# Kernel optimization log

Hardware: AMD Instinct MI355X
Metric: run time of the kernel (lower is better)

## Reference

```python
import jax, jax.numpy as jnp
import numpy as np

N, E, IN, ED, HID, B, K = 50000, 800000, 128, 64, 256, 128, 1000


def setup_inputs() -> dict:
    key = jax.random.key(0)
    ks = jax.random.split(key, 16)

    def lin(k, fi, fo):
        k1, k2 = jax.random.split(k)
        s = 1.0 / np.sqrt(fi)
        return (jax.random.uniform(k1, (fi, fo), jnp.float32, -s, s),
                jax.random.uniform(k2, (fo,), jnp.float32, -s, s))

    We, be = lin(ks[0], ED, IN)        # GINEConv edge projection edge_dim -> in_channels
    W1, b1 = lin(ks[1], IN, HID)       # GINE nn layer 1
    W2, b2 = lin(ks[2], HID, HID)      # GINE nn layer 2
    Wg1, bg1 = lin(ks[3], HID, 128)    # gate_nn layer 1
    Wg2, bg2 = lin(ks[4], 128, 1)      # gate_nn layer 2
    Wh, bh = lin(ks[5], HID, K)        # head

    x = jax.random.normal(ks[6], (N, IN), jnp.float32)
    edge_index = jax.random.randint(ks[7], (2, E), 0, N, jnp.int64)
    edge_attr = jax.random.normal(ks[8], (E, ED), jnp.float32)
    batch = jnp.sort(jax.random.randint(ks[9], (N,), 0, B, jnp.int64))

    return {"x": x, "edge_index": edge_index, "edge_attr": edge_attr, "batch": batch,
            "We": We, "be": be, "W1": W1, "b1": b1, "W2": W2, "b2": b2,
            "Wg1": Wg1, "bg1": bg1, "Wg2": Wg2, "bg2": bg2, "Wh": Wh, "bh": bh}


def reference(x, edge_index, edge_attr, batch, We, be, W1, b1, W2, b2,
              Wg1, bg1, Wg2, bg2, Wh, bh):
    src, dst = edge_index[0], edge_index[1]
    # GINEConv message: ReLU(x_j + Lin(edge_attr)), scatter-add to dst (eps=0)
    e = edge_attr @ We + be                      # [E, IN]
    m = jax.nn.relu(x[src] + e)                  # [E, IN]
    agg = jax.ops.segment_sum(m, dst, num_segments=N)  # [N, IN]
    h = x + agg                                  # (1+eps)*x + agg, eps=0
    h = jax.nn.relu(h @ W1 + b1) @ W2 + b2       # [N, HID]
    # GlobalAttention: segment softmax of gate over graphs, weighted sum
    gate = jax.nn.relu(h @ Wg1 + bg1) @ Wg2 + bg2            # [N, 1]
    gmax = jax.ops.segment_max(gate, batch, num_segments=B)  # [B, 1]
    a = jnp.exp(gate - gmax[batch])
    denom = jax.ops.segment_sum(a, batch, num_segments=B)    # [B, 1]
    attn = a / denom[batch]
    pooled = jax.ops.segment_sum(attn * h, batch, num_segments=B)  # [B, HID]
    logits = pooled @ Wh + bh                    # [B, K]
    return (logits, pooled)
```

## Files before the change

### kernel.cpp

```cpp
#include <hip/hip_runtime.h>
#include <stdint.h>

#define NN    50000
#define EE    800000
#define IN_C  128
#define ED_C  64
#define HID_C 256
#define BB    128
#define KK    1000
#define G1_C  128
#define NV    50176


typedef __attribute__((ext_vector_type(8))) short bfrag;
typedef __attribute__((ext_vector_type(4))) float f4acc;

__device__ __forceinline__ unsigned short f2bs(float f){
  unsigned u = __float_as_uint(f);
  return (unsigned short)((u + 0x7fffu + ((u >> 16) & 1u)) >> 16);
}
__device__ __forceinline__ float bs2f(unsigned short s){
  return __uint_as_float(((unsigned)s) << 16);
}

__device__ __forceinline__ void atomicMaxFloat(float* addr, float val){
  int old = __float_as_int(*addr);
  while (__int_as_float(old) < val){
    int assumed = old;
    old = atomicCAS((int*)addr, assumed, __float_as_int(val));
    if (old == assumed) break;
  }
}

__global__ __launch_bounds__(256) void k_prep(
    const float* __restrict__ We, const float* __restrict__ W1,
    const float* __restrict__ W2, const float* __restrict__ Wg1,
    unsigned short* __restrict__ Wet, unsigned short* __restrict__ W1t,
    unsigned short* __restrict__ W2t, unsigned short* __restrict__ Wg1t)
{
  int i = blockIdx.x * 256 + threadIdx.x;
  if (i < 128 * 64){ int c = i >> 6, k = i & 63;  Wet[i]  = f2bs(We[k * 128 + c]); }
  if (i < 256 * 128){ int n = i >> 7, k = i & 127; W1t[i]  = f2bs(W1[k * 256 + n]); }
  if (i < 256 * 256){ int n = i >> 8, k = i & 255; W2t[i]  = f2bs(W2[k * 256 + n]); }
  if (i < 128 * 256){ int n = i >> 8, k = i & 255; Wg1t[i] = f2bs(Wg1[k * 128 + n]); }
}

__global__ __launch_bounds__(256) void k_init(float* __restrict__ agg,
                                              int* __restrict__ cnt,
                                              int* __restrict__ fill,
                                              int* __restrict__ aux,
                                              float* __restrict__ gmax,
                                              float* __restrict__ denom,
                                              float* __restrict__ pooled){
  size_t i = (size_t)blockIdx.x * 256 + threadIdx.x;
  if (i < (size_t)NN * IN_C) agg[i] = 0.f;
  if (i < NV){ cnt[i] = 0; fill[i] = 0; }
  if (i < 256) aux[i] = 0;
  if (i < BB){ gmax[i] = -1e30f; denom[i] = 0.f; }
  if (i < BB * HID_C) pooled[i] = 0.f;
}

__global__ __launch_bounds__(256) void k_hist(const int* __restrict__ ei,
                                              int* __restrict__ cnt){
  int e = blockIdx.x * 256 + threadIdx.x;
  if (e < EE) atomicAdd(&cnt[ei[EE + e]], 1);
}

__global__ __launch_bounds__(256) void k_scan1(const int* __restrict__ cnt,
                                               int* __restrict__ off,
                                               int* __restrict__ aux){
  __shared__ int s[256];
  int t = threadIdx.x, i = blockIdx.x * 256 + t;
  int val = cnt[i];
  s[t] = val; __syncthreads();
#pragma unroll
  for (int o = 1; o < 256; o <<= 1){
    int v = (t >= o) ? s[t - o] : 0;
    __syncthreads();
    s[t] += v;
    __syncthreads();
  }
  off[i] = s[t] - val;
  if (t == 255) aux[blockIdx.x] = s[255];
}

__global__ __launch_bounds__(256) void k_scan2(int* __restrict__ aux){
  __shared__ int s[256];
  int t = threadIdx.x;
  int val = aux[t];
  s[t] = val; __syncthreads();
#pragma unroll
  for (int o = 1; o < 256; o <<= 1){
    int v = (t >= o) ? s[t - o] : 0;
    __syncthreads();
    s[t] += v;
    __syncthreads();
  }
  aux[t] = s[t] - val;
}

__global__ __launch_bounds__(256) void k_scan3(int* __restrict__ off,
                                               const int* __restrict__ aux){
  int i = blockIdx.x * 256 + threadIdx.x;
  off[i] += aux[blockIdx.x];
}

__global__ __launch_bounds__(256) void k_scatter(const int* __restrict__ ei,
                                                 const int* __restrict__ off,
                                                 int* __restrict__ fill,
                                                 uint4* __restrict__ sorted){
  int e = blockIdx.x * 256 + threadIdx.x;
  if (e < EE){
    int s = ei[e], d = ei[EE + e];
    int pos = off[d] + atomicAdd(&fill[d], 1);
    sorted[pos] = make_uint4((unsigned)e, (unsigned)s, (unsigned)d, 0u);
  }
}

__global__ __launch_bounds__(256, 4) void k_edge2(
    const float* __restrict__ x, const uint4* __restrict__ sorted,
    const float* __restrict__ edge_attr,
    const unsigned short* __restrict__ Wet, const float* __restrict__ be,
    float* __restrict__ agg)
{
  __shared__ float msgS[64 * 132];
  __shared__ uint4 sE[64];
  __shared__ int runStart[66];
  __shared__ int nRunsS;
  unsigned short* eaS = (unsigned short*)msgS;

  const int tid = threadIdx.x;
  const int e0 = blockIdx.x * 64;
  if (tid < 64) sE[tid] = sorted[e0 + tid];
  __syncthreads();

  const int lane = tid & 63, wv = tid >> 6;
  const int q = lane >> 4, l15 = lane & 15;
  const int g0 = wv * 16;

  const int xrow = g0 + (lane >> 2);
  const int xc0 = (lane & 3) * 32;
  const float* xptr = x + (size_t)((int)sE[xrow].y) * IN_C + xc0;
  float4 xr[8];
#pragma unroll
  for (int j = 0; j < 8; ++j) xr[j] = *(const float4*)(xptr + j * 4);

#pragma unroll
  for (int t = 0; t < 4; ++t){
    int f4 = t * 256 + tid;
    int er = f4 >> 4;
    int kk = (f4 & 15) * 4;
    int eid = (int)sE[er].x;
    const float4 v = *(const float4*)(edge_attr + (size_t)eid * ED_C + kk);
    unsigned p0 = (unsigned)f2bs(v.x) | ((unsigned)f2bs(v.y) << 16);
    unsigned p1 = (unsigned)f2bs(v.z) | ((unsigned)f2bs(v.w) << 16);
    *(uint2*)&eaS[er * 72 + kk] = make_uint2(p0, p1);
  }

  if (tid < 64){
    bool flag = (tid == 0) || ((int)sE[tid].z != (int)sE[tid - 1].z);
    unsigned long long m = __ballot(flag);
    int pre = __popcll(m & ((1ull << tid) - 1ull));
    if ((m >> tid) & 1ull) runStart[pre] = tid;
    if (tid == 0){
      int nr = __popcll(m);
      nRunsS = nr;
      runStart[nr] = 64;
    }
  }
  __syncthreads();

  f4acc acc[8];
  const f4acc zz = {0.f, 0.f, 0.f, 0.f};
#pragma unroll
  for (int nt = 0; nt < 8; ++nt) acc[nt] = zz;

#pragma unroll
  for (int ks = 0; ks < 2; ++ks){
    bfrag a = *(const bfrag*)&eaS[(g0 + l15) * 72 + ks * 32 + q * 8];
#pragma unroll
    for (int nt = 0; nt < 8; ++nt){
      int c = nt * 16 + l15;
      bfrag b = *(const bfrag*)(Wet + c * ED_C + ks * 32 + q * 8);
      acc[nt] = __builtin_amdgcn_mfma_f32_16x16x32_bf16(a, b, acc[nt], 0, 0, 0);
    }
  }

  float bev[8];
#pragma unroll
  for (int nt = 0; nt < 8; ++nt) bev[nt] = be[nt * 16 + l15];

  __syncthreads();

#pragma unroll
  for (int nt = 0; nt < 8; ++nt){
    int c = nt * 16 + l15;
#pragma unroll
    for (int r = 0; r < 4; ++r)
      msgS[(g0 + q * 4 + r) * 132 + c] = acc[nt][r] + bev[nt];
  }

  {
    float* mr = &msgS[xrow * 132 + xc0];
#pragma unroll
    for (int j = 0; j < 8; ++j){
      float4 w = *(float4*)(mr + j * 4);
      const float4 v = xr[j];
      w.x = fmaxf(w.x + v.x, 0.f);
      w.y = fmaxf(w.y + v.y, 0.f);
      w.z = fmaxf(w.z + v.z, 0.f);
      w.w = fmaxf(w.w + v.w, 0.f);
      *(float4*)(mr + j * 4) = w;
    }
  }
  __syncthreads();

  {
    const int col = tid & 127;
    const int h = tid >> 7;
    const int nR = nRunsS;
    for (int i = h; i < nR; i += 2){
      int s = runStart[i], e = runStart[i + 1];
      int dst = (int)sE[s].z;
      float run = 0.f;
      for (int r = s; r < e; ++r) run += msgS[r * 132 + col];
      size_t a = (size_t)dst * IN_C + col;
      if (s == 0 || e == 64) atomicAdd(&agg[a], run);
      else                   agg[a] = run;
    }
  }
}

__global__ __launch_bounds__(256) void k_h0(const float* __restrict__ agg,
                                            const float* __restrict__ x,
                                            unsigned short* __restrict__ h0b){
  int i = blockIdx.x * 256 + threadIdx.x;
  if (i < NN * IN_C) h0b[i] = f2bs(agg[i] + x[i]);
}

template<int K, bool RELU, bool OF32, bool OB16>
__global__ __launch_bounds__(256) void k_gemm(
    const unsigned short* __restrict__ A, const unsigned short* __restrict__ Wt,
    const float* __restrict__ bias, float* __restrict__ outf,
    unsigned short* __restrict__ outb, int M, int Ntot)
{
  __shared__ unsigned short aS[64 * 40];
  __shared__ unsigned short bS[128 * 40];
  const int tid = threadIdx.x;
  const int lane = tid & 63, wv = tid >> 6;
  const int wi = wv >> 1, wj = wv & 1;
  const int q = lane >> 4, l15 = lane & 15;
  const int mb0 = blockIdx.x * 64;
  const int nb0 = blockIdx.y * 128;
  const int arow = tid >> 2, achk = tid & 3;

  f4acc acc[2][4];
  const f4acc zz = {0.f, 0.f, 0.f, 0.f};
#pragma unroll
  for (int mt = 0; mt < 2; ++mt)
#pragma unroll
    for (int nt = 0; nt < 4; ++nt) acc[mt][nt] = zz;

  for (int ks = 0; ks < K / 32; ++ks){
    {
      int m = mb0 + arow; if (m >= M) m = M - 1;
      const uint4 v = *(const uint4*)(A + (size_t)m * K + ks * 32 + achk * 8);
      *(uint4*)&aS[arow * 40 + achk * 8] = v;
    }
#pragma unroll
    for (int i = 0; i < 2; ++i){
      int idx = i * 256 + tid;
      int row = idx >> 2, chk = idx & 3;
      const uint4 v = *(const uint4*)(Wt + (size_t)(nb0 + row) * K + ks * 32 + chk * 8);
      *(uint4*)&bS[row * 40 + chk * 8] = v;
    }
    __syncthreads();
    bfrag a[2], b[4];
#pragma unroll
    for (int mt = 0; mt < 2; ++mt)
      a[mt] = *(const bfrag*)&aS[(wi * 32 + mt * 16 + l15) * 40 + q * 8];
#pragma unroll
    for (int nt = 0; nt < 4; ++nt)
      b[nt] = *(const bfrag*)&bS[(wj * 64 + nt * 16 + l15) * 40 + q * 8];
#pragma unroll
    for (int mt = 0; mt < 2; ++mt)
#pragma unroll
      for (int nt = 0; nt < 4; ++nt)
        acc[mt][nt] = __builtin_amdgcn_mfma_f32_16x16x32_bf16(a[mt], b[nt], acc[mt][nt], 0, 0, 0);
    __syncthreads();
  }

  const int mb = mb0 + wi * 32;
  const int nb = nb0 + wj * 64;
#pragma unroll
  for (int nt = 0; nt < 4; ++nt){
    int c = nb + nt * 16 + l15;
    float bv = bias[c];
#pragma unroll
    for (int mt = 0; mt < 2; ++mt){
#pragma unroll
      for (int r = 0; r < 4; ++r){
        int m = mb + mt * 16 + q * 4 + r;
        if (m < M){
          float v = acc[mt][nt][r] + bv;
          if (RELU) v = v > 0.f ? v : 0.f;
          if (OF32) outf[(size_t)m * Ntot + c] = v;
          if (OB16) outb[(size_t)m * Ntot + c] = f2bs(v);
        }
      }
    }
  }
}

__global__ __launch_bounds__(256) void k_gate2(const float* __restrict__ g1,
                                               const float* __restrict__ Wg2,
                                               const float* __restrict__ bg2,
                                               float* __restrict__ gate, int nrows){
  const int lane = threadIdx.x & 63, wv = threadIdx.x >> 6;
  const float2 w2 = *(const float2*)(Wg2 + lane * 2);
  const float bg = bg2[0];
  for (int r = blockIdx.x * 4 + wv; r < nrows; r += gridDim.x * 4){
    const float2 a2 = *(const float2*)(g1 + (size_t)r * G1_C + lane * 2);
    float p = a2.x * w2.x + a2.y * w2.y;
#pragma unroll
    for (int off = 32; off > 0; off >>= 1) p += __shfl_down(p, off);
    if (lane == 0) gate[r] = p + bg;
  }
}

__global__ __launch_bounds__(256) void k_gmax(const float* __restrict__ gate,
                                              const int* __restrict__ batch,
                                              float* __restrict__ gmax, int nrows){
  __shared__ float red[256];
  const int tid = threadIdx.x;
  const int n0 = blockIdx.x * 256;
  const int n = n0 + tid;
  const int nlast = (n0 + 255 < nrows) ? n0 + 255 : nrows - 1;
  const int bmin = batch[n0], bmax = batch[nlast];
  float val = -3e38f; int b = bmax;
  if (n < nrows){ b = batch[n]; val = gate[n]; }
  for (int bb = bmin; bb <= bmax; ++bb){
    red[tid] = (b == bb) ? val : -3e38f;
    __syncthreads();
    for (int s = 128; s > 0; s >>= 1){
      if (tid < s) red[tid] = fmaxf(red[tid], red[tid + s]);
      __syncthreads();
    }
    if (tid == 0 && red[0] > -1e37f) atomicMaxFloat(&gmax[bb], red[0]);
    __syncthreads();
  }
}

__global__ __launch_bounds__(256) void k_expsum(const float* __restrict__ gate,
                                                const int* __restrict__ batch,
                                                const float* __restrict__ gmax,
                                                float* __restrict__ aexp,
                                                float* __restrict__ denom, int nrows){
  __shared__ float red[256];
  const int tid = threadIdx.x;
  const int n0 = blockIdx.x * 256;
  const int n = n0 + tid;
  const int nlast = (n0 + 255 < nrows) ? n0 + 255 : nrows - 1;
  const int bmin = batch[n0], bmax = batch[nlast];
  float val = 0.f; int b = bmax;
  if (n < nrows){
    b = batch[n];
    val = expf(gate[n] - gmax[b]);
    aexp[n] = val;
  }
  for (int bb = bmin; bb <= bmax; ++bb){
    red[tid] = (b == bb) ? val : 0.f;
    __syncthreads();
    for (int s = 128; s > 0; s >>= 1){
      if (tid < s) red[tid] += red[tid + s];
      __syncthreads();
    }
    if (tid == 0 && red[0] != 0.f) atomicAdd(&denom[bb], red[0]);
    __syncthreads();
  }
}

__global__ __launch_bounds__(256) void k_pool(const unsigned short* __restrict__ h2b,
                                              const float* __restrict__ aexp,
                                              const float* __restrict__ denom,
                                              const int* __restrict__ batch,
                                              float* __restrict__ pooled, int nrows){
  const int c = threadIdx.x;
  const int n0 = blockIdx.x * 256;
  int n1 = n0 + 256; if (n1 > nrows) n1 = nrows;
  float acc = 0.f;
  int curb = batch[n0];
  for (int n = n0; n < n1; ++n){
    int b = batch[n];
    if (b != curb){
      atomicAdd(&pooled[(size_t)curb * HID_C + c], acc);
      acc = 0.f; curb = b;
    }
    float wgt = aexp[n] / denom[b];
    acc = fmaf(wgt, bs2f(h2b[(size_t)n * HID_C + c]), acc);
  }
  atomicAdd(&pooled[(size_t)curb * HID_C + c], acc);
}

__global__ __launch_bounds__(256) void k_head(const float* __restrict__ pooled,
                                              const float* __restrict__ Wh,
                                              const float* __restrict__ bh,
                                              float* __restrict__ out_logits,
                                              float* __restrict__ out_pooled){
  __shared__ float p[HID_C];
  const int b = blockIdx.x, t = threadIdx.x;
  float pv = pooled[(size_t)b * HID_C + t];
  p[t] = pv;
  out_pooled[(size_t)b * HID_C + t] = pv;
  __syncthreads();
  for (int c = t; c < KK; c += 256){
    float acc = bh[c];
#pragma unroll 8
    for (int k = 0; k < HID_C; ++k)
      acc = fmaf(p[k], Wh[k * KK + c], acc);
    out_logits[(size_t)b * KK + c] = acc;
  }
}

extern "C" void kernel_launch(void* const* d_in, const int* in_sizes, int n_in,
                              void* d_out, int out_size, void* d_ws, size_t ws_size,
                              hipStream_t stream) {
  const float* x   = (const float*)d_in[0];
  const int*   ei  = (const int*)d_in[1];
  const float* ea  = (const float*)d_in[2];
  const int*   batch = (const int*)d_in[3];
  const float* We  = (const float*)d_in[4];
  const float* be  = (const float*)d_in[5];
  const float* W1  = (const float*)d_in[6];
  const float* b1  = (const float*)d_in[7];
  const float* W2  = (const float*)d_in[8];
  const float* b2  = (const float*)d_in[9];
  const float* Wg1 = (const float*)d_in[10];
  const float* bg1 = (const float*)d_in[11];
  const float* Wg2 = (const float*)d_in[12];
  const float* bg2 = (const float*)d_in[13];
  const float* Wh  = (const float*)d_in[14];
  const float* bh  = (const float*)d_in[15];

  float* out_logits = (float*)d_out;
  float* out_pooled = out_logits + (size_t)BB * KK;

  float* agg    = (float*)d_ws;
  float* gate   = agg   + (size_t)NN * IN_C;
  float* aexp   = gate  + NN;
  float* gmax   = aexp  + NN;
  float* denom  = gmax  + BB;
  float* pooled = denom + BB;
  float* fend   = pooled + (size_t)BB * HID_C;
  unsigned short* h0b  = (unsigned short*)fend;
  unsigned short* h1b  = h0b + (size_t)NN * IN_C;
  unsigned short* h2b  = h1b + (size_t)NN * HID_C;
  unsigned short* Wet  = h2b + (size_t)NN * HID_C;
  unsigned short* W1t  = Wet + 128 * 64;
  unsigned short* W2t  = W1t + 256 * 128;
  unsigned short* Wg1t = W2t + 256 * 256;
  float* g1f = agg;
  uint4* sorted = (uint4*)h1b;
  int* cnt  = (int*)(sorted + EE);
  int* off  = cnt + NV;
  int* fill = off + NV;
  int* aux  = fill + NV;

  k_prep<<<256, 256, 0, stream>>>(We, W1, W2, Wg1, Wet, W1t, W2t, Wg1t);
  k_init<<<(NN * IN_C + 255) / 256, 256, 0, stream>>>(agg, cnt, fill, aux, gmax, denom, pooled);
  k_hist   <<<(EE + 255) / 256, 256, 0, stream>>>(ei, cnt);
  k_scan1  <<<NV / 256, 256, 0, stream>>>(cnt, off, aux);
  k_scan2  <<<1, 256, 0, stream>>>(aux);
  k_scan3  <<<NV / 256, 256, 0, stream>>>(off, aux);
  k_scatter<<<(EE + 255) / 256, 256, 0, stream>>>(ei, off, fill, sorted);
  k_edge2<<<EE / 64, 256, 0, stream>>>(x, sorted, ea, Wet, be, agg);
  k_h0<<<(NN * IN_C + 255) / 256, 256, 0, stream>>>(agg, x, h0b);
  k_gemm<128, true,  false, true ><<<dim3(782, 2), 256, 0, stream>>>(h0b, W1t, b1, (float*)0, h1b, NN, HID_C);
  k_gemm<256, false, false, true ><<<dim3(782, 2), 256, 0, stream>>>(h1b, W2t, b2, (float*)0, h2b, NN, HID_C);
  k_gemm<256, true,  true,  false><<<dim3(782, 1), 256, 0, stream>>>(h2b, Wg1t, bg1, g1f, (unsigned short*)0, NN, G1_C);
  k_gate2<<<3125, 256, 0, stream>>>(g1f, Wg2, bg2, gate, NN);
  k_gmax  <<<(NN + 255) / 256, 256, 0, stream>>>(gate, batch, gmax, NN);
  k_expsum<<<(NN + 255) / 256, 256, 0, stream>>>(gate, batch, gmax, aexp, denom, NN);
  k_pool  <<<(NN + 255) / 256, 256, 0, stream>>>(h2b, aexp, denom, batch, pooled, NN);
  k_head<<<BB, 256, 0, stream>>>(pooled, Wh, bh, out_logits, out_pooled);
}
```

Baseline: 751.0 us.

## Pre-permute edge attributes to bf16 in destination-sorted order during scatter

The scatter pass now writes each edge's attributes, converted to bf16, into a destination-sorted buffer alongside a compact (src,dst) pair. The edge-message kernel then reads the attribute tile contiguously, with no per-edge fp32 gather or conversion inside the MFMA projection. This removes the indirect fp32 edge_attr reads from the edge kernel, but adds an extra full-size bf16 write and read of the edge attributes. The new path runs only when the workspace is large enough; otherwise the old path is kept.

```diff
diff --git a/kernel.cpp b/kernel.cpp
--- a/kernel.cpp
+++ b/kernel.cpp
@@ -117,6 +117,26 @@
   }
 }
 
+__global__ __launch_bounds__(256) void k_scatter2(
+    const int* __restrict__ ei, const float* __restrict__ ea,
+    const int* __restrict__ off, int* __restrict__ fill,
+    uint2* __restrict__ sd, unsigned short* __restrict__ EA)
+{
+  int e = blockIdx.x * 256 + threadIdx.x;
+  if (e >= EE) return;
+  int s = ei[e], d = ei[EE + e];
+  int pos = off[d] + atomicAdd(&fill[d], 1);
+  sd[pos] = make_uint2((unsigned)s, (unsigned)d);
+  const float4* s4 = (const float4*)(ea + (size_t)e * ED_C);
+  uint2* d2 = (uint2*)(EA + (size_t)pos * ED_C);
+#pragma unroll
+  for (int j = 0; j < 16; ++j){
+    float4 v = s4[j];
+    d2[j] = make_uint2((unsigned)f2bs(v.x) | ((unsigned)f2bs(v.y) << 16),
+                       (unsigned)f2bs(v.z) | ((unsigned)f2bs(v.w) << 16));
+  }
+}
+
 __global__ __launch_bounds__(256, 4) void k_edge2(
     const float* __restrict__ x, const uint4* __restrict__ sorted,
     const float* __restrict__ edge_attr,
@@ -222,6 +242,104 @@
     for (int i = h; i < nR; i += 2){
       int s = runStart[i], e = runStart[i + 1];
       int dst = (int)sE[s].z;
+      float run = 0.f;
+      for (int r = s; r < e; ++r) run += msgS[r * 132 + col];
+      size_t a = (size_t)dst * IN_C + col;
+      if (s == 0 || e == 64) atomicAdd(&agg[a], run);
+      else                   agg[a] = run;
+    }
+  }
+}
+
+__global__ __launch_bounds__(256, 4) void k_edge3(
+    const float* __restrict__ x, const uint2* __restrict__ sd,
+    const unsigned short* __restrict__ EA,
+    const unsigned short* __restrict__ Wet, const float* __restrict__ be,
+    float* __restrict__ agg)
+{
+  __shared__ float msgS[64 * 132];
+  __shared__ uint2 sE[64];
+  __shared__ int runStart[66];
+  __shared__ int nRunsS;
+
+  const int tid = threadIdx.x;
+  if (tid < 64) sE[tid] = sd[(size_t)blockIdx.x * 64 + tid];
+  __syncthreads();
+
+  const int lane = tid & 63, wv = tid >> 6;
+  const int q = lane >> 4, l15 = lane & 15;
+  const int g0 = wv * 16;
+
+  const int xrow = g0 + (lane >> 2);
+  const int xc0 = (lane & 3) * 32;
+  const float* xptr = x + (size_t)((int)sE[xrow].x) * IN_C + xc0;
+  float4 xr[8];
+#pragma unroll
+  for (int j = 0; j < 8; ++j) xr[j] = *(const float4*)(xptr + j * 4);
+
+  if (tid < 64){
+    bool flag = (tid == 0) || (sE[tid].y != sE[tid - 1].y);
+    unsigned long long m = __ballot(flag);
+    int pre = __popcll(m & ((1ull << tid) - 1ull));
+    if ((m >> tid) & 1ull) runStart[pre] = tid;
+    if (tid == 0){
+      int nr = __popcll(m);
+      nRunsS = nr;
+      runStart[nr] = 64;
+    }
+  }
+
+  const unsigned short* EAb = EA + (size_t)blockIdx.x * 64 * ED_C;
+  f4acc acc[8];
+  const f4acc zz = {0.f, 0.f, 0.f, 0.f};
+#pragma unroll
+  for (int nt = 0; nt < 8; ++nt) acc[nt] = zz;
+
+#pragma unroll
+  for (int ks = 0; ks < 2; ++ks){
+    bfrag a = *(const bfrag*)(EAb + (size_t)(g0 + l15) * ED_C + ks * 32 + q * 8);
+#pragma unroll
+    for (int nt = 0; nt < 8; ++nt){
+      int c = nt * 16 + l15;
+      bfrag b = *(const bfrag*)(Wet + c * ED_C + ks * 32 + q * 8);
+      acc[nt] = __builtin_amdgcn_mfma_f32_16x16x32_bf16(a, b, acc[nt], 0, 0, 0);
+    }
+  }
+
+  float bev[8];
+#pragma unroll
+  for (int nt = 0; nt < 8; ++nt) bev[nt] = be[nt * 16 + l15];
+
+#pragma unroll
+  for (int nt = 0; nt < 8; ++nt){
+    int c = nt * 16 + l15;
+#pragma unroll
+    for (int r = 0; r < 4; ++r)
+      msgS[(g0 + q * 4 + r) * 132 + c] = acc[nt][r] + bev[nt];
+  }
+
+  {
+    float* mr = &msgS[xrow * 132 + xc0];
+#pragma unroll
+    for (int j = 0; j < 8; ++j){
+      float4 w = *(float4*)(mr + j * 4);
+      const float4 v = xr[j];
+      w.x = fmaxf(w.x + v.x, 0.f);
+      w.y = fmaxf(w.y + v.y, 0.f);
+      w.z = fmaxf(w.z + v.z, 0.f);
+      w.w = fmaxf(w.w + v.w, 0.f);
+      *(float4*)(mr + j * 4) = w;
+    }
+  }
+  __syncthreads();
+
+  {
+    const int col = tid & 127;
+    const int h = tid >> 7;
+    const int nR = nRunsS;
+    for (int i = h; i < nR; i += 2){
+      int s = runStart[i], e = runStart[i + 1];
+      int dst = (int)sE[s].y;
       float run = 0.f;
       for (int r = s; r < e; ++r) run += msgS[r * 132 + col];
       size_t a = (size_t)dst * IN_C + col;
@@ -452,35 +570,75 @@
   float* denom  = gmax  + BB;
   float* pooled = denom + BB;
   float* fend   = pooled + (size_t)BB * HID_C;
-  unsigned short* h0b  = (unsigned short*)fend;
-  unsigned short* h1b  = h0b + (size_t)NN * IN_C;
-  unsigned short* h2b  = h1b + (size_t)NN * HID_C;
-  unsigned short* Wet  = h2b + (size_t)NN * HID_C;
-  unsigned short* W1t  = Wet + 128 * 64;
-  unsigned short* W2t  = W1t + 256 * 128;
-  unsigned short* Wg1t = W2t + 256 * 256;
   float* g1f = agg;
-  uint4* sorted = (uint4*)h1b;
-  int* cnt  = (int*)(sorted + EE);
-  int* off  = cnt + NV;
-  int* fill = off + NV;
-  int* aux  = fill + NV;
-
-  k_prep<<<256, 256, 0, stream>>>(We, W1, W2, Wg1, Wet, W1t, W2t, Wg1t);
-  k_init<<<(NN * IN_C + 255) / 256, 256, 0, stream>>>(agg, cnt, fill, aux, gmax, denom, pooled);
-  k_hist   <<<(EE + 255) / 256, 256, 0, stream>>>(ei, cnt);
-  k_scan1  <<<NV / 256, 256, 0, stream>>>(cnt, off, aux);
-  k_scan2  <<<1, 256, 0, stream>>>(aux);
-  k_scan3  <<<NV / 256, 256, 0, stream>>>(off, aux);
-  k_scatter<<<(EE + 255) / 256, 256, 0, stream>>>(ei, off, fill, sorted);
-  k_edge2<<<EE / 64, 256, 0, stream>>>(x, sorted, ea, Wet, be, agg);
-  k_h0<<<(NN * IN_C + 255) / 256, 256, 0, stream>>>(agg, x, h0b);
-  k_gemm<128, true,  false, true ><<<dim3(782, 2), 256, 0, stream>>>(h0b, W1t, b1, (float*)0, h1b, NN, HID_C);
-  k_gemm<256, false, false, true ><<<dim3(782, 2), 256, 0, stream>>>(h1b, W2t, b2, (float*)0, h2b, NN, HID_C);
-  k_gemm<256, true,  true,  false><<<dim3(782, 1), 256, 0, stream>>>(h2b, Wg1t, bg1, g1f, (unsigned short*)0, NN, G1_C);
-  k_gate2<<<3125, 256, 0, stream>>>(g1f, Wg2, bg2, gate, NN);
-  k_gmax  <<<(NN + 255) / 256, 256, 0, stream>>>(gate, batch, gmax, NN);
-  k_expsum<<<(NN + 255) / 256, 256, 0, stream>>>(gate, batch, gmax, aexp, denom, NN);
-  k_pool  <<<(NN + 255) / 256, 256, 0, stream>>>(h2b, aexp, denom, batch, pooled, NN);
-  k_head<<<BB, 256, 0, stream>>>(pooled, Wh, bh, out_logits, out_pooled);
-}
+
+  const size_t NEED_BIG = 136000000ULL;
+
+  if (ws_size >= NEED_BIG){
+    unsigned short* Wet  = (unsigned short*)fend;
+    unsigned short* W1t  = Wet + 128 * 64;
+    unsigned short* W2t  = W1t + 256 * 128;
+    unsigned short* Wg1t = W2t + 256 * 256;
+    unsigned short* wend = Wg1t + 128 * 256;
+    uint2* sd = (uint2*)wend;
+    int* cnt  = (int*)(sd + EE);
+    int* off  = cnt + NV;
+    int* fill = off + NV;
+    int* aux  = fill + NV;
+    size_t o = (size_t)((char*)(aux + 256) - (char*)d_ws);
+    o = (o + 15) & ~(size_t)15;
+    unsigned short* h0b = (unsigned short*)((char*)d_ws + o);
+    unsigned short* EA  = h0b;
+    unsigned short* h1b = h0b + (size_t)NN * IN_C;
+    unsigned short* h2b = h1b + (size_t)NN * HID_C;
+
+    k_prep<<<256, 256, 0, stream>>>(We, W1, W2, Wg1, Wet, W1t, W2t, Wg1t);
+    k_init<<<(NN * IN_C + 255) / 256, 256, 0, stream>>>(agg, cnt, fill, aux, gmax, denom, pooled);
+    k_hist   <<<(EE + 255) / 256, 256, 0, stream>>>(ei, cnt);
+    k_scan1  <<<NV / 256, 256, 0, stream>>>(cnt, off, aux);
+    k_scan2  <<<1, 256, 0, stream>>>(aux);
+    k_scan3  <<<NV / 256, 256, 0, stream>>>(off, aux);
+    k_scatter2<<<(EE + 255) / 256, 256, 0, stream>>>(ei, ea, off, fill, sd, EA);
+    k_edge3<<<EE / 64, 256, 0, stream>>>(x, sd, EA, Wet, be, agg);
+    k_h0<<<(NN * IN_C + 255) / 256, 256, 0, stream>>>(agg, x, h0b);
+    k_gemm<128, true,  false, true ><<<dim3(782, 2), 256, 0, stream>>>(h0b, W1t, b1, (float*)0, h1b, NN, HID_C);
+    k_gemm<256, false, false, true ><<<dim3(782, 2), 256, 0, stream>>>(h1b, W2t, b2, (float*)0, h2b, NN, HID_C);
+    k_gemm<256, true,  true,  false><<<dim3(782, 1), 256, 0, stream>>>(h2b, Wg1t, bg1, g1f, (unsigned short*)0, NN, G1_C);
+    k_gate2<<<3125, 256, 0, stream>>>(g1f, Wg2, bg2, gate, NN);
+    k_gmax  <<<(NN + 255) / 256, 256, 0, stream>>>(gate, batch, gmax, NN);
+    k_expsum<<<(NN + 255) / 256, 256, 0, stream>>>(gate, batch, gmax, aexp, denom, NN);
+    k_pool  <<<(NN + 255) / 256, 256, 0, stream>>>(h2b, aexp, denom, batch, pooled, NN);
+    k_head<<<BB, 256, 0, stream>>>(pooled, Wh, bh, out_logits, out_pooled);
+  } else {
+    unsigned short* h0b  = (unsigned short*)fend;
+    unsigned short* h1b  = h0b + (size_t)NN * IN_C;
+    unsigned short* h2b  = h1b + (size_t)NN * HID_C;
+    unsigned short* Wet  = h2b + (size_t)NN * HID_C;
+    unsigned short* W1t  = Wet + 128 * 64;
+    unsigned short* W2t  = W1t + 256 * 128;
+    unsigned short* Wg1t = W2t + 256 * 256;
+    uint4* sorted = (uint4*)h1b;
+    int* cnt  = (int*)(sorted + EE);
+    int* off  = cnt + NV;
+    int* fill = off + NV;
+    int* aux  = fill + NV;
+
+    k_prep<<<256, 256, 0, stream>>>(We, W1, W2, Wg1, Wet, W1t, W2t, Wg1t);
+    k_init<<<(NN * IN_C + 255) / 256, 256, 0, stream>>>(agg, cnt, fill, aux, gmax, denom, pooled);
+    k_hist   <<<(EE + 255) / 256, 256, 0, stream>>>(ei, cnt);
+    k_scan1  <<<NV / 256, 256, 0, stream>>>(cnt, off, aux);
+    k_scan2  <<<1, 256, 0, stream>>>(aux);
+    k_scan3  <<<NV / 256, 256, 0, stream>>>(off, aux);
+    k_scatter<<<(EE + 255) / 256, 256, 0, stream>>>(ei, off, fill, sorted);
+    k_edge2<<<EE / 64, 256, 0, stream>>>(x, sorted, ea, Wet, be, agg);
+    k_h0<<<(NN * IN_C + 255) / 256, 256, 0, stream>>>(agg, x, h0b);
+    k_gemm<128, true,  false, true ><<<dim3(782, 2), 256, 0, stream>>>(h0b, W1t, b1, (float*)0, h1b, NN, HID_C);
+    k_gemm<256, false, false, true ><<<dim3(782, 2), 256, 0, stream>>>(h1b, W2t, b2, (float*)0, h2b, NN, HID_C);
+    k_gemm<256, true,  true,  false><<<dim3(782, 1), 256, 0, stream>>>(h2b, Wg1t, bg1, g1f, (unsigned short*)0, NN, G1_C);
+    k_gate2<<<3125, 256, 0, stream>>>(g1f, Wg2, bg2, gate, NN);
+    k_gmax  <<<(NN + 255) / 256, 256, 0, stream>>>(gate, batch, gmax, NN);
+    k_expsum<<<(NN + 255) / 256, 256, 0, stream>>>(gate, batch, gmax, aexp, denom, NN);
+    k_pool  <<<(NN + 255) / 256, 256, 0, stream>>>(h2b, aexp, denom, batch, pooled, NN);
+    k_head<<<BB, 256, 0, stream>>>(pooled, Wh, bh, out_logits, out_pooled);
+  }
+}
```

Result: slower. 814.5 us (+8.5%).
